# Kernel tuning notes

Measured on AMD Instinct MI355X. Metric: run time of the kernel, lower is better.

Reference implementation:

```python
import jax, jax.numpy as jnp
import numpy as np

PATCH_LENGTH = 200

def setup_inputs() -> dict:
    key = jax.random.key(0)
    eeg_input = jax.random.normal(key, (16, 32, 1000, 64), dtype=jnp.float32)
    return {"eeg_input": eeg_input}

def reference(eeg_input):
    # eeg_input: [B, W, T, C]
    B, W, T, C = eeg_input.shape
    nt = T // PATCH_LENGTH  # number of time patches per channel
    T_used = nt * PATCH_LENGTH
    # Torch loops iterate ch_idx (outer), t_idx (inner) -> channel-major patch order.
    # [B, W, T, C] -> [B, W, C, T] -> [B, W, C, nt, P] -> [B, W, C*nt, P]
    x = jnp.transpose(eeg_input[:, :, :T_used, :], (0, 1, 3, 2))
    patches = x.reshape(B, W, C * nt, PATCH_LENGTH)
    channel_indices = jnp.repeat(jnp.arange(C, dtype=jnp.int64), nt)  # [C*nt]
    time_indices = jnp.tile(jnp.arange(nt, dtype=jnp.int64), C)       # [C*nt]
    return patches, channel_indices, time_indices
```

## Files before the change

### kernel.cpp

```cpp
#include <hip/hip_runtime.h>


#define TDIM 1000
#define PATCH_ELEMS 32768000

__global__ __launch_bounds__(256, 8) void labram_patcher_kernel(
    const float* __restrict__ in, float* __restrict__ out)
{
    __shared__ float lds[4 * TDIM];

    const int tid  = threadIdx.x;
    const int phys = blockIdx.x;
    const int virt = (phys & 7) * 1024 + (phys >> 3);
    const int bw = virt >> 4;
    const int cq = virt & 15;

    const float4* gsrc = (const float4*)in + (size_t)bw * 16000 + cq;

    float4 v[4];
    #pragma unroll
    for (int k = 0; k < 3; ++k)
        v[k] = gsrc[(size_t)(tid + k * 256) * 16];
    const int t3 = tid + 768;
    if (t3 < TDIM)
        v[3] = gsrc[(size_t)t3 * 16];

    #pragma unroll
    for (int k = 0; k < 4; ++k) {
        const int t = tid + k * 256;
        if (k < 3 || t < TDIM) {
            lds[            t] = v[k].x;
            lds[    TDIM +  t] = v[k].y;
            lds[2 * TDIM +  t] = v[k].z;
            lds[3 * TDIM +  t] = v[k].w;
        }
    }
    __syncthreads();

    const float4* lds4 = (const float4*)lds;
    float4* dst = (float4*)out + (size_t)bw * 16000 + (size_t)cq * 1000;

    #pragma unroll
    for (int k = 0; k < 4; ++k) {
        const int i = tid + k * 256;
        if (k < 3 || i < 1000)
            dst[i] = lds4[i];
    }

    if (phys == 0) {
        for (int i = tid; i < 320; i += 256) {
            out[PATCH_ELEMS + i]       = (float)(i / 5);
            out[PATCH_ELEMS + 320 + i] = (float)(i % 5);
        }
    }
}

extern "C" void kernel_launch(void* const* d_in, const int* in_sizes, int n_in,
                              void* d_out, int out_size, void* d_ws, size_t ws_size,
                              hipStream_t stream) {
    const float* in = (const float*)d_in[0];
    float* out = (float*)d_out;
    dim3 grid(512 * 16);
    dim3 block(256);
    labram_patcher_kernel<<<grid, block, 0, stream>>>(in, out);
}
```

Measured before the change: 241.1 us.

## Tile transpose by time blocks with padded LDS instead of channel quads

Each block now handles a 64-timestep by 64-channel tile instead of 4 channels across all 1000 timesteps. Global reads become fully contiguous 1KB rows, where before they were 16-byte strided gathers. The tile is transposed through an LDS buffer padded to a stride of 65 to avoid bank conflicts. Output writes become 256-byte row segments per channel instead of a full contiguous 4KB run, and LDS reads are scalar rather than float4.

After: 241.3 us. No clear change (+0.1%).

```diff
diff --git a/kernel.cpp b/kernel.cpp
--- a/kernel.cpp
+++ b/kernel.cpp
@@ -2,49 +2,63 @@
 
 
 #define TDIM 1000
+#define CDIM 64
+#define LSTR 65
 #define PATCH_ELEMS 32768000
 
 __global__ __launch_bounds__(256, 8) void labram_patcher_kernel(
     const float* __restrict__ in, float* __restrict__ out)
 {
-    __shared__ float lds[4 * TDIM];
+    __shared__ float lds[CDIM * LSTR];
 
     const int tid  = threadIdx.x;
     const int phys = blockIdx.x;
     const int virt = (phys & 7) * 1024 + (phys >> 3);
     const int bw = virt >> 4;
-    const int cq = virt & 15;
+    const int ti = virt & 15;
+    const int t0 = (ti < 15) ? ti * 64 : 960;
+    const int nt = (ti < 15) ? 64 : 40;
 
-    const float4* gsrc = (const float4*)in + (size_t)bw * 16000 + cq;
+    const float4* src4 = (const float4*)in + (size_t)bw * 16000 + (size_t)t0 * 16;
 
     float4 v[4];
-    #pragma unroll
-    for (int k = 0; k < 3; ++k)
-        v[k] = gsrc[(size_t)(tid + k * 256) * 16];
-    const int t3 = tid + 768;
-    if (t3 < TDIM)
-        v[3] = gsrc[(size_t)t3 * 16];
-
+    int tr[4];
     #pragma unroll
     for (int k = 0; k < 4; ++k) {
-        const int t = tid + k * 256;
-        if (k < 3 || t < TDIM) {
-            lds[            t] = v[k].x;
-            lds[    TDIM +  t] = v[k].y;
-            lds[2 * TDIM +  t] = v[k].z;
-            lds[3 * TDIM +  t] = v[k].w;
+        const int i = tid + k * 256;
+        tr[k] = i >> 4;
+        if (tr[k] < nt)
+            v[k] = src4[tr[k] * 16 + (i & 15)];
+    }
+    #pragma unroll
+    for (int k = 0; k < 4; ++k) {
+        const int i = tid + k * 256;
+        const int u = i & 15;
+        if (tr[k] < nt) {
+            lds[(4 * u + 0) * LSTR + tr[k]] = v[k].x;
+            lds[(4 * u + 1) * LSTR + tr[k]] = v[k].y;
+            lds[(4 * u + 2) * LSTR + tr[k]] = v[k].z;
+            lds[(4 * u + 3) * LSTR + tr[k]] = v[k].w;
         }
     }
     __syncthreads();
 
-    const float4* lds4 = (const float4*)lds;
-    float4* dst = (float4*)out + (size_t)bw * 16000 + (size_t)cq * 1000;
+    float4* dst4 = (float4*)out + (size_t)bw * 16000 + (t0 >> 2);
 
     #pragma unroll
     for (int k = 0; k < 4; ++k) {
         const int i = tid + k * 256;
-        if (k < 3 || i < 1000)
-            dst[i] = lds4[i];
+        const int c = i >> 4;
+        const int u = i & 15;
+        if (4 * u < nt) {
+            const int b = c * LSTR + 4 * u;
+            float4 w;
+            w.x = lds[b + 0];
+            w.y = lds[b + 1];
+            w.z = lds[b + 2];
+            w.w = lds[b + 3];
+            dst4[(size_t)c * 250 + u] = w;
+        }
     }
 
     if (phys == 0) {
```
